# Optimization experiments

Hardware: AMD Instinct MI355X
Metric: run time of the kernel (lower is better)

## Reference

```python
import math
import jax, jax.numpy as jnp
import numpy as np

B, T, C, H = 2, 2048, 1024, 16
HD = C // H

def gelu_tanh(x):
    # 0.5*x*(1+tanh(sqrt(2/pi)*(x+0.044715*x^3)))
    c = math.sqrt(2.0 / math.pi)
    return 0.5 * x * (1.0 + jnp.tanh(c * (x + 0.044715 * x * x * x)))

def layernorm(x, g, b, eps=1e-5):
    mu = jnp.mean(x, axis=-1, keepdims=True)
    var = jnp.var(x, axis=-1, keepdims=True)
    return (x - mu) * jax.lax.rsqrt(var + eps) * g + b

def setup_inputs() -> dict:
    key = jax.random.key(0)
    ks = jax.random.split(key, 6)
    s = 0.02
    return {
        "x": jax.random.normal(ks[0], (B, T, C), jnp.float32),
        "ln1_g": jnp.ones((C,), jnp.float32),
        "ln1_b": jnp.zeros((C,), jnp.float32),
        "W_qkv": jax.random.normal(ks[1], (C, 3 * C), jnp.float32) * s,
        "b_qkv": jnp.zeros((3 * C,), jnp.float32),
        "W_out": jax.random.normal(ks[2], (C, C), jnp.float32) * s,
        "b_out": jnp.zeros((C,), jnp.float32),
        "ln2_g": jnp.ones((C,), jnp.float32),
        "ln2_b": jnp.zeros((C,), jnp.float32),
        "W_fc1": jax.random.normal(ks[3], (C, 4 * C), jnp.float32) * s,
        "b_fc1": jnp.zeros((4 * C,), jnp.float32),
        "W_fc2": jax.random.normal(ks[4], (4 * C, C), jnp.float32) * s,
        "b_fc2": jnp.zeros((C,), jnp.float32),
    }

def reference(x, ln1_g, ln1_b, W_qkv, b_qkv, W_out, b_out,
              ln2_g, ln2_b, W_fc1, b_fc1, W_fc2, b_fc2):
    # pre-LN causal self-attention
    h = layernorm(x, ln1_g, ln1_b)
    qkv = h @ W_qkv + b_qkv                      # [B,T,3C]
    q, k, v = jnp.split(qkv, 3, axis=-1)
    q = q.reshape(B, T, H, HD).transpose(0, 2, 1, 3)  # [B,H,T,HD]
    k = k.reshape(B, T, H, HD).transpose(0, 2, 1, 3)
    v = v.reshape(B, T, H, HD).transpose(0, 2, 1, 3)
    scores = jnp.einsum("bhqd,bhkd->bhqk", q, k) * (1.0 / math.sqrt(HD))
    causal = jnp.tril(jnp.ones((T, T), bool))
    scores = jnp.where(causal, scores, jnp.float32(-jnp.inf))
    att = jax.nn.softmax(scores, axis=-1)
    out = jnp.einsum("bhqk,bhkd->bhqd", att, v)  # [B,H,T,HD]
    out = out.transpose(0, 2, 1, 3).reshape(B, T, C)
    out = out @ W_out + b_out
    temp = x + out
    # GELU MLP
    h2 = layernorm(temp, ln2_g, ln2_b)
    ff = gelu_tanh(h2 @ W_fc1 + b_fc1) @ W_fc2 + b_fc2
    return temp + ff
```

## Files before the change

### kernel.cpp

```cpp
#include <hip/hip_runtime.h>
#include <stdint.h>

#define Bb 2
#define Tt 2048
#define Cc 1024
#define Hh 16
#define HD 64
#define Mm (Bb*Tt)

typedef __bf16 bf16x8 __attribute__((ext_vector_type(8)));
typedef float  f32x4  __attribute__((ext_vector_type(4)));

#define DEV static __device__ __forceinline__

DEV float asfloat_(uint32_t u){ union{uint32_t u; float f;} x; x.u=u; return x.f; }
DEV uint32_t asuint_(float f){ union{float f; uint32_t u;} x; x.f=f; return x.u; }
DEV unsigned short f2bf(float f){
  uint32_t u = asuint_(f);
  uint32_t r = (u + 0x7fffu + ((u>>16)&1u)) >> 16;
  return (unsigned short)r;
}
DEV float gelu_(float x){
  float x3 = x*x*x;
  float t  = 0.7978845608028654f * (x + 0.044715f*x3);
  float e  = __expf(2.0f*t);
  float th = 1.0f - 2.0f/(e + 1.0f);
  return 0.5f * x * (1.0f + th);
}

__global__ void wcvt_kernel(const float* __restrict__ W, unsigned short* __restrict__ WT,
                            int K, int N) {
  __shared__ float tile[32][33];
  int tx = threadIdx.x & 31, ty = threadIdx.x >> 5;
  int kb = blockIdx.x * 32, nb = blockIdx.y * 32;
  #pragma unroll
  for (int r = 0; r < 32; r += 8)
    tile[ty + r][tx] = W[(size_t)(kb + ty + r) * N + nb + tx];
  __syncthreads();
  #pragma unroll
  for (int r = 0; r < 32; r += 8)
    WT[(size_t)(nb + ty + r) * K + kb + tx] = f2bf(tile[tx][ty + r]);
}

__global__ void ln_kernel(const float* __restrict__ X, const float* __restrict__ g,
                          const float* __restrict__ bb, unsigned short* __restrict__ O) {
  int row = blockIdx.x, t = threadIdx.x;
  const float4* xr = (const float4*)(X + (size_t)row * Cc);
  float4 v = xr[t];
  float s = v.x + v.y + v.z + v.w;
  float q = v.x*v.x + v.y*v.y + v.z*v.z + v.w*v.w;
  #pragma unroll
  for (int o = 32; o > 0; o >>= 1) { s += __shfl_xor(s, o); q += __shfl_xor(q, o); }
  __shared__ float ss[4], sq[4];
  int w = t >> 6;
  if ((t & 63) == 0) { ss[w] = s; sq[w] = q; }
  __syncthreads();
  s = ss[0] + ss[1] + ss[2] + ss[3];
  q = sq[0] + sq[1] + sq[2] + sq[3];
  float mu  = s * (1.0f/Cc);
  float var = q * (1.0f/Cc) - mu*mu;
  float rstd = rsqrtf(var + 1e-5f);
  float4 gv = ((const float4*)g)[t], bv = ((const float4*)bb)[t];
  ushort4 o4;
  o4.x = f2bf((v.x-mu)*rstd*gv.x + bv.x);
  o4.y = f2bf((v.y-mu)*rstd*gv.y + bv.y);
  o4.z = f2bf((v.z-mu)*rstd*gv.z + bv.z);
  o4.w = f2bf((v.w-mu)*rstd*gv.w + bv.w);
  ((ushort4*)(O + (size_t)row * Cc))[t] = o4;
}

template<int MODE>
__launch_bounds__(256, 2)
__global__ void gemm_kernel(const unsigned short* __restrict__ A,
                            const unsigned short* __restrict__ BT,
                            const float* __restrict__ bias,
                            const float* __restrict__ res,
                            void* __restrict__ Cout,
                            int N, int K) {
  __shared__ unsigned short As[128*32];
  __shared__ unsigned short Bs[128*32];
  int tid  = threadIdx.x;
  int lane = tid & 63, w = tid >> 6;
  int wr = w >> 1, wc = w & 1;
  int bm = blockIdx.x, bn = blockIdx.y;

  f32x4 acc[4][4];
  #pragma unroll
  for (int m = 0; m < 4; ++m)
    #pragma unroll
    for (int n = 0; n < 4; ++n) acc[m][n] = (f32x4){0.f,0.f,0.f,0.f};

  int arow   = tid >> 2;
  int kchunk = (tid & 3) * 8;
  const unsigned short* Ag = A  + (size_t)(bm*128 + arow) * K + kchunk;
  const unsigned short* Bg = BT + (size_t)(bn*128 + arow) * K + kchunk;
  int nk = K >> 5;

  for (int kt = 0; kt < nk; ++kt) {
    if (kt) __syncthreads();
    const unsigned short* ag = Ag + kt*32;
    const unsigned short* bg = Bg + kt*32;
    __builtin_amdgcn_global_load_lds((const __attribute__((address_space(1))) void*)ag,
        (__attribute__((address_space(3))) void*)(As + w*512), 16, 0, 0);
    __builtin_amdgcn_global_load_lds((const __attribute__((address_space(1))) void*)(ag + (size_t)64*K),
        (__attribute__((address_space(3))) void*)(As + 2048 + w*512), 16, 0, 0);
    __builtin_amdgcn_global_load_lds((const __attribute__((address_space(1))) void*)bg,
        (__attribute__((address_space(3))) void*)(Bs + w*512), 16, 0, 0);
    __builtin_amdgcn_global_load_lds((const __attribute__((address_space(1))) void*)(bg + (size_t)64*K),
        (__attribute__((address_space(3))) void*)(Bs + 2048 + w*512), 16, 0, 0);
    __syncthreads();

    bf16x8 af[4], bfr[4];
    #pragma unroll
    for (int m = 0; m < 4; ++m)
      af[m] = *(const bf16x8*)(As + (wr*64 + m*16 + (lane&15))*32 + (lane>>4)*8);
    #pragma unroll
    for (int n = 0; n < 4; ++n)
      bfr[n] = *(const bf16x8*)(Bs + (wc*64 + n*16 + (lane&15))*32 + (lane>>4)*8);
    #pragma unroll
    for (int m = 0; m < 4; ++m)
      #pragma unroll
      for (int n = 0; n < 4; ++n)
        acc[m][n] = __builtin_amdgcn_mfma_f32_16x16x32_bf16(af[m], bfr[n], acc[m][n], 0, 0, 0);
  }

  int r0 = bm*128 + wr*64;
  int c0 = bn*128 + wc*64;
  int lr = (lane >> 4) * 4;
  int lc = lane & 15;
  #pragma unroll
  for (int m = 0; m < 4; ++m) {
    #pragma unroll
    for (int n = 0; n < 4; ++n) {
      int col = c0 + n*16 + lc;
      float bv = bias[col];
      #pragma unroll
      for (int i = 0; i < 4; ++i) {
        int row = r0 + m*16 + lr + i;
        float v = acc[m][n][i] + bv;
        if (MODE == 1 || MODE == 3) v += res[(size_t)row * N + col];
        if (MODE == 2) v = gelu_(v);
        if (MODE == 0 || MODE == 2)
          ((unsigned short*)Cout)[(size_t)row * N + col] = f2bf(v);
        else
          ((float*)Cout)[(size_t)row * N + col] = v;
      }
    }
  }
}

__global__ void vtr_kernel(const unsigned short* __restrict__ qkv,
                           unsigned short* __restrict__ vtb) {
  __shared__ unsigned short Tl[64][72];
  int tid = threadIdx.x;
  int bh = blockIdx.x, tc = blockIdx.y;
  int b = bh >> 4, h = bh & 15;
  int r = tid >> 2, c0 = (tid & 3) * 16;
  const unsigned short* src = qkv + (size_t)(b*Tt + tc*64 + r)*3072 + 2048 + h*64 + c0;
  *(int4*)&Tl[r][c0]     = *(const int4*)(src);
  *(int4*)&Tl[r][c0 + 8] = *(const int4*)(src + 8);
  __syncthreads();
  int d = tid >> 2, k0 = (tid & 3) * 16;
  ushort4 o[4];
  #pragma unroll
  for (int jj = 0; jj < 4; ++jj) {
    o[jj].x = Tl[k0 + jj*4 + 0][d];
    o[jj].y = Tl[k0 + jj*4 + 1][d];
    o[jj].z = Tl[k0 + jj*4 + 2][d];
    o[jj].w = Tl[k0 + jj*4 + 3][d];
  }
  unsigned short* dst = vtb + ((size_t)(bh*64 + d))*2048 + tc*64 + k0;
  *(int4*)(dst)     = *(int4*)&o[0];
  *(int4*)(dst + 8) = *(int4*)&o[2];
}

__global__ __launch_bounds__(512, 4)
void attn_kernel(const unsigned short* __restrict__ qkv,
                 const unsigned short* __restrict__ vtb,
                 unsigned short* __restrict__ att) {
  __shared__ __align__(16) char smem[36864];
  int tid  = threadIdx.x;
  int lane = tid & 63, w = tid >> 6;
  int g = lane >> 4, ql = lane & 15;

  int bid = blockIdx.x;
  int bh = bid & 31;
  int jj = bid >> 5;
  int j  = (jj < 8) ? (2*jj) : (31 - 2*jj);
  int b = bh >> 4, h = bh & 15;
  int Q0 = j * 128;
  int qbase = Q0 + w * 16;
  char* Pb = smem + 16384 + w * 2560;

  const unsigned short* qrow = qkv + (size_t)(b*Tt + qbase + ql) * 3072 + h*64;
  bf16x8 qf0 = *(const bf16x8*)(qrow + g*8);
  bf16x8 qf1 = *(const bf16x8*)(qrow + 32 + g*8);

  f32x4 O[4];
  #pragma unroll
  for (int d = 0; d < 4; ++d) O[d] = (f32x4){0.f,0.f,0.f,0.f};
  float mrun = -1e30f, lrun = 0.f;

  int nt = Q0/64 + 2;

  int srow = tid >> 3;
  int scol = (tid & 7) * 8;
  int wr_off = srow*128 + ((scol*2) ^ ((srow & 7) << 4));
  const unsigned short* Kg = qkv + (size_t)(b*Tt + srow)*3072 + 1024 + h*64 + scol;
  const unsigned short* Vg = vtb + ((size_t)(bh*64 + srow))*2048 + scol;

  int4 kreg = *(const int4*)(Kg);
  int4 vreg = *(const int4*)(Vg);

  for (int t0 = 0; t0 < nt; ++t0) {
    __syncthreads();
    *(int4*)(smem + wr_off)        = kreg;
    *(int4*)(smem + 8192 + wr_off) = vreg;
    __syncthreads();
    if (t0 + 1 < nt) {
      kreg = *(const int4*)(Kg + (size_t)(t0+1)*64*3072);
      vreg = *(const int4*)(Vg + (t0+1)*64);
    }
    if (t0*64 > qbase + 15) continue;

    bool full = (t0*64 + 63) <= qbase;
    float ps[16];
    #pragma unroll
    for (int s = 0; s < 4; ++s) {
      int krow = s*16 + ql;
      int kb0 = krow*128 + (( g*16      ) ^ ((krow&7)<<4));
      int kb1 = krow*128 + (( g*16 + 64 ) ^ ((krow&7)<<4));
      bf16x8 kf0 = *(const bf16x8*)(smem + kb0);
      bf16x8 kf1 = *(const bf16x8*)(smem + kb1);
      f32x4 a = (f32x4){0.f,0.f,0.f,0.f};
      a = __builtin_amdgcn_mfma_f32_16x16x32_bf16(kf0, qf0, a, 0, 0, 0);
      a = __builtin_amdgcn_mfma_f32_16x16x32_bf16(kf1, qf1, a, 0, 0, 0);
      #pragma unroll
      for (int i = 0; i < 4; ++i) ps[s*4+i] = a[i] * 0.125f;
    }
    if (!full) {
      #pragma unroll
      for (int s = 0; s < 4; ++s)
        #pragma unroll
        for (int i = 0; i < 4; ++i)
          if (t0*64 + s*16 + g*4 + i > qbase + ql) ps[s*4+i] = -1e30f;
    }
    float tm = ps[0];
    #pragma unroll
    for (int i = 1; i < 16; ++i) tm = fmaxf(tm, ps[i]);
    tm = fmaxf(tm, __shfl_xor(tm, 16));
    tm = fmaxf(tm, __shfl_xor(tm, 32));
    float mnew = fmaxf(mrun, tm);
    float corr = __expf(mrun - mnew);
    float tsum = 0.f;
    #pragma unroll
    for (int s = 0; s < 4; ++s) {
      float e0 = __expf(ps[s*4+0] - mnew);
      float e1 = __expf(ps[s*4+1] - mnew);
      float e2 = __expf(ps[s*4+2] - mnew);
      float e3 = __expf(ps[s*4+3] - mnew);
      tsum += (e0 + e1) + (e2 + e3);
      ushort4 pk;
      pk.x = f2bf(e0); pk.y = f2bf(e1); pk.z = f2bf(e2); pk.w = f2bf(e3);
      *(ushort4*)(Pb + ql*160 + s*32 + g*8) = pk;
    }
    tsum += __shfl_xor(tsum, 16);
    tsum += __shfl_xor(tsum, 32);
    lrun = lrun * corr + tsum;
    mrun = mnew;

    float c0 = __shfl(corr, g*4 + 0);
    float c1 = __shfl(corr, g*4 + 1);
    float c2 = __shfl(corr, g*4 + 2);
    float c3 = __shfl(corr, g*4 + 3);
    #pragma unroll
    for (int d = 0; d < 4; ++d) {
      O[d][0] *= c0; O[d][1] *= c1; O[d][2] *= c2; O[d][3] *= c3;
    }
    #pragma unroll
    for (int kk = 0; kk < 2; ++kk) {
      bf16x8 pf = *(const bf16x8*)(Pb + ql*160 + kk*64 + g*16);
      #pragma unroll
      for (int d = 0; d < 4; ++d) {
        int drow = d*16 + ql;
        int vb = drow*128 + ((kk*64 + g*16) ^ ((drow&7)<<4));
        bf16x8 vf = *(const bf16x8*)(smem + 8192 + vb);
        O[d] = __builtin_amdgcn_mfma_f32_16x16x32_bf16(pf, vf, O[d], 0, 0, 0);
      }
    }
  }

  float l0 = __shfl(lrun, g*4 + 0);
  float l1 = __shfl(lrun, g*4 + 1);
  float l2 = __shfl(lrun, g*4 + 2);
  float l3 = __shfl(lrun, g*4 + 3);
  #pragma unroll
  for (int d = 0; d < 4; ++d) {
    size_t base = (size_t)(b*Tt + qbase)*Cc + h*64 + d*16 + ql;
    att[base + (size_t)(g*4+0)*Cc] = f2bf(O[d][0] / l0);
    att[base + (size_t)(g*4+1)*Cc] = f2bf(O[d][1] / l1);
    att[base + (size_t)(g*4+2)*Cc] = f2bf(O[d][2] / l2);
    att[base + (size_t)(g*4+3)*Cc] = f2bf(O[d][3] / l3);
  }
}

extern "C" void kernel_launch(void* const* d_in, const int* in_sizes, int n_in,
                              void* d_out, int out_size, void* d_ws, size_t ws_size,
                              hipStream_t stream) {
  const float* x    = (const float*)d_in[0];
  const float* ln1g = (const float*)d_in[1];
  const float* ln1b = (const float*)d_in[2];
  const float* Wqkv = (const float*)d_in[3];
  const float* bqkv = (const float*)d_in[4];
  const float* Wout = (const float*)d_in[5];
  const float* bout = (const float*)d_in[6];
  const float* ln2g = (const float*)d_in[7];
  const float* ln2b = (const float*)d_in[8];
  const float* Wfc1 = (const float*)d_in[9];
  const float* bfc1 = (const float*)d_in[10];
  const float* Wfc2 = (const float*)d_in[11];
  const float* bfc2 = (const float*)d_in[12];

  char* ws = (char*)d_ws;
  unsigned short* wqkvT = (unsigned short*)(ws);
  unsigned short* woutT = (unsigned short*)(ws + (6u<<20));
  unsigned short* wfc1T = (unsigned short*)(ws + (8u<<20));
  unsigned short* wfc2T = (unsigned short*)(ws + (16u<<20));
  unsigned short* vtb   = (unsigned short*)(ws + (24u<<20));
  float*          temp  = (float*)(ws + (24u<<20));
  unsigned short* hbuf  = (unsigned short*)(ws + (40u<<20));
  unsigned short* qkvb  = (unsigned short*)(ws + (48u<<20));
  unsigned short* attb  = (unsigned short*)(ws + (72u<<20));
  unsigned short* a1b   = (unsigned short*)(ws + (48u<<20));

  dim3 b256(256);
  wcvt_kernel<<<dim3(1024/32, 3072/32), b256, 0, stream>>>(Wqkv, wqkvT, 1024, 3072);
  wcvt_kernel<<<dim3(1024/32, 1024/32), b256, 0, stream>>>(Wout, woutT, 1024, 1024);
  wcvt_kernel<<<dim3(1024/32, 4096/32), b256, 0, stream>>>(Wfc1, wfc1T, 1024, 4096);
  wcvt_kernel<<<dim3(4096/32, 1024/32), b256, 0, stream>>>(Wfc2, wfc2T, 4096, 1024);

  ln_kernel<<<Mm, b256, 0, stream>>>(x, ln1g, ln1b, hbuf);
  gemm_kernel<0><<<dim3(Mm/128, 3072/128), b256, 0, stream>>>(hbuf, wqkvT, bqkv, nullptr, qkvb, 3072, 1024);
  vtr_kernel<<<dim3(32, 32), b256, 0, stream>>>(qkvb, vtb);
  attn_kernel<<<dim3(512), 512, 0, stream>>>(qkvb, vtb, attb);
  gemm_kernel<1><<<dim3(Mm/128, 1024/128), b256, 0, stream>>>(attb, woutT, bout, x, temp, 1024, 1024);
  ln_kernel<<<Mm, b256, 0, stream>>>(temp, ln2g, ln2b, hbuf);
  gemm_kernel<2><<<dim3(Mm/128, 4096/128), b256, 0, stream>>>(hbuf, wfc1T, bfc1, nullptr, a1b, 4096, 1024);
  gemm_kernel<3><<<dim3(Mm/128, 1024/128), b256, 0, stream>>>(a1b, wfc2T, bfc2, temp, d_out, 1024, 4096);
}
```

Before: 375.3 us.

## Widen GEMM K-tile to 64 with XOR-swizzled LDS and 8-wave blocks

The GEMM kernel now uses 512-thread blocks (8 waves in a 2x4 arrangement), each wave computing 64x32 instead of 64x64. The K tile grows from 32 to 64, halving the number of load/sync iterations. Global-to-LDS loads place 16-byte chunks with an XOR swizzle so fragment reads avoid bank conflicts. This trades fewer barriers and better LDS access for more waves per block and a larger LDS footprint, while still keeping a single LDS buffer with no double buffering.

```diff
diff --git a/kernel.cpp b/kernel.cpp
--- a/kernel.cpp
+++ b/kernel.cpp
@@ -27,6 +27,10 @@
   float th = 1.0f - 2.0f/(e + 1.0f);
   return 0.5f * x * (1.0f + th);
 }
+
+#define GLL(gsrc, ldst) __builtin_amdgcn_global_load_lds( \
+    (const __attribute__((address_space(1))) void*)(gsrc), \
+    (__attribute__((address_space(3))) void*)(ldst), 16, 0, 0)
 
 __global__ void wcvt_kernel(const float* __restrict__ W, unsigned short* __restrict__ WT,
                             int K, int N) {
@@ -70,69 +74,71 @@
 }
 
 template<int MODE>
-__launch_bounds__(256, 2)
+__launch_bounds__(512, 4)
 __global__ void gemm_kernel(const unsigned short* __restrict__ A,
                             const unsigned short* __restrict__ BT,
                             const float* __restrict__ bias,
                             const float* __restrict__ res,
                             void* __restrict__ Cout,
                             int N, int K) {
-  __shared__ unsigned short As[128*32];
-  __shared__ unsigned short Bs[128*32];
+  __shared__ unsigned short As[128*64];
+  __shared__ unsigned short Bs[128*64];
   int tid  = threadIdx.x;
   int lane = tid & 63, w = tid >> 6;
-  int wr = w >> 1, wc = w & 1;
+  int wr = w >> 2, wc = w & 3;
+  int g = lane >> 4, ql = lane & 15;
   int bm = blockIdx.x, bn = blockIdx.y;
 
-  f32x4 acc[4][4];
+  f32x4 acc[4][2];
   #pragma unroll
   for (int m = 0; m < 4; ++m)
     #pragma unroll
-    for (int n = 0; n < 4; ++n) acc[m][n] = (f32x4){0.f,0.f,0.f,0.f};
-
-  int arow   = tid >> 2;
-  int kchunk = (tid & 3) * 8;
-  const unsigned short* Ag = A  + (size_t)(bm*128 + arow) * K + kchunk;
-  const unsigned short* Bg = BT + (size_t)(bn*128 + arow) * K + kchunk;
-  int nk = K >> 5;
+    for (int n = 0; n < 2; ++n) acc[m][n] = (f32x4){0.f,0.f,0.f,0.f};
+
+  int r  = tid >> 3;
+  int cc = tid & 7;
+  int sc = (cc ^ (r & 7)) * 8;
+  const unsigned short* Ag = A  + (size_t)(bm*128 + r) * K + sc;
+  const unsigned short* Bg = BT + (size_t)(bn*128 + r) * K + sc;
+  int sw = (ql & 7) << 3;
+  int nk = K >> 6;
 
   for (int kt = 0; kt < nk; ++kt) {
     if (kt) __syncthreads();
-    const unsigned short* ag = Ag + kt*32;
-    const unsigned short* bg = Bg + kt*32;
-    __builtin_amdgcn_global_load_lds((const __attribute__((address_space(1))) void*)ag,
-        (__attribute__((address_space(3))) void*)(As + w*512), 16, 0, 0);
-    __builtin_amdgcn_global_load_lds((const __attribute__((address_space(1))) void*)(ag + (size_t)64*K),
-        (__attribute__((address_space(3))) void*)(As + 2048 + w*512), 16, 0, 0);
-    __builtin_amdgcn_global_load_lds((const __attribute__((address_space(1))) void*)bg,
-        (__attribute__((address_space(3))) void*)(Bs + w*512), 16, 0, 0);
-    __builtin_amdgcn_global_load_lds((const __attribute__((address_space(1))) void*)(bg + (size_t)64*K),
-        (__attribute__((address_space(3))) void*)(Bs + 2048 + w*512), 16, 0, 0);
+    const unsigned short* ag = Ag + kt*64;
+    const unsigned short* bg = Bg + kt*64;
+    GLL(ag,                  As + w*512);
+    GLL(ag + (size_t)64*K,   As + 4096 + w*512);
+    GLL(bg,                  Bs + w*512);
+    GLL(bg + (size_t)64*K,   Bs + 4096 + w*512);
     __syncthreads();
 
-    bf16x8 af[4], bfr[4];
-    #pragma unroll
-    for (int m = 0; m < 4; ++m)
-      af[m] = *(const bf16x8*)(As + (wr*64 + m*16 + (lane&15))*32 + (lane>>4)*8);
-    #pragma unroll
-    for (int n = 0; n < 4; ++n)
-      bfr[n] = *(const bf16x8*)(Bs + (wc*64 + n*16 + (lane&15))*32 + (lane>>4)*8);
-    #pragma unroll
-    for (int m = 0; m < 4; ++m)
-      #pragma unroll
-      for (int n = 0; n < 4; ++n)
-        acc[m][n] = __builtin_amdgcn_mfma_f32_16x16x32_bf16(af[m], bfr[n], acc[m][n], 0, 0, 0);
+    #pragma unroll
+    for (int kk = 0; kk < 2; ++kk) {
+      int col = (kk*32 + g*8) ^ sw;
+      bf16x8 af[4], bf2[2];
+      #pragma unroll
+      for (int m = 0; m < 4; ++m)
+        af[m] = *(const bf16x8*)(As + (wr*64 + m*16 + ql)*64 + col);
+      #pragma unroll
+      for (int n = 0; n < 2; ++n)
+        bf2[n] = *(const bf16x8*)(Bs + (wc*32 + n*16 + ql)*64 + col);
+      #pragma unroll
+      for (int m = 0; m < 4; ++m)
+        #pragma unroll
+        for (int n = 0; n < 2; ++n)
+          acc[m][n] = __builtin_amdgcn_mfma_f32_16x16x32_bf16(af[m], bf2[n], acc[m][n], 0, 0, 0);
+    }
   }
 
   int r0 = bm*128 + wr*64;
-  int c0 = bn*128 + wc*64;
-  int lr = (lane >> 4) * 4;
-  int lc = lane & 15;
+  int c0 = bn*128 + wc*32;
+  int lr = g * 4;
   #pragma unroll
   for (int m = 0; m < 4; ++m) {
     #pragma unroll
-    for (int n = 0; n < 4; ++n) {
-      int col = c0 + n*16 + lc;
+    for (int n = 0; n < 2; ++n) {
+      int col = c0 + n*16 + ql;
       float bv = bias[col];
       #pragma unroll
       for (int i = 0; i < 4; ++i) {
@@ -333,18 +339,18 @@
   unsigned short* attb  = (unsigned short*)(ws + (72u<<20));
   unsigned short* a1b   = (unsigned short*)(ws + (48u<<20));
 
-  dim3 b256(256);
+  dim3 b256(256), b512(512);
   wcvt_kernel<<<dim3(1024/32, 3072/32), b256, 0, stream>>>(Wqkv, wqkvT, 1024, 3072);
   wcvt_kernel<<<dim3(1024/32, 1024/32), b256, 0, stream>>>(Wout, woutT, 1024, 1024);
   wcvt_kernel<<<dim3(1024/32, 4096/32), b256, 0, stream>>>(Wfc1, wfc1T, 1024, 4096);
   wcvt_kernel<<<dim3(4096/32, 1024/32), b256, 0, stream>>>(Wfc2, wfc2T, 4096, 1024);
 
   ln_kernel<<<Mm, b256, 0, stream>>>(x, ln1g, ln1b, hbuf);
-  gemm_kernel<0><<<dim3(Mm/128, 3072/128), b256, 0, stream>>>(hbuf, wqkvT, bqkv, nullptr, qkvb, 3072, 1024);
+  gemm_kernel<0><<<dim3(Mm/128, 3072/128), b512, 0, stream>>>(hbuf, wqkvT, bqkv, nullptr, qkvb, 3072, 1024);
   vtr_kernel<<<dim3(32, 32), b256, 0, stream>>>(qkvb, vtb);
   attn_kernel<<<dim3(512), 512, 0, stream>>>(qkvb, vtb, attb);
-  gemm_kernel<1><<<dim3(Mm/128, 1024/128), b256, 0, stream>>>(attb, woutT, bout, x, temp, 1024, 1024);
+  gemm_kernel<1><<<dim3(Mm/128, 1024/128), b512, 0, stream>>>(attb, woutT, bout, x, temp, 1024, 1024);
   ln_kernel<<<Mm, b256, 0, stream>>>(temp, ln2g, ln2b, hbuf);
-  gemm_kernel<2><<<dim3(Mm/128, 4096/128), b256, 0, stream>>>(hbuf, wfc1T, bfc1, nullptr, a1b, 4096, 1024);
-  gemm_kernel<3><<<dim3(Mm/128, 1024/128), b256, 0, stream>>>(a1b, wfc2T, bfc2, temp, d_out, 1024, 4096);
-}
+  gemm_kernel<2><<<dim3(Mm/128, 4096/128), b512, 0, stream>>>(hbuf, wfc1T, bfc1, nullptr, a1b, 4096, 1024);
+  gemm_kernel<3><<<dim3(Mm/128, 1024/128), b512, 0, stream>>>(a1b, wfc2T, bfc2, temp, d_out, 1024, 4096);
+}
```

Measured after the change: 368.4 us. Within noise of the previous version (-1.8%).
